# Kernel tuning notes

Hardware: AMD Instinct MI355X
Metric: run time of the kernel (lower is better)

Reference implementation:

```python
import jax, jax.numpy as jnp
import numpy as np

N_POINTS = 100000
N_EVENTS = 1000000
N_PAIRS = 100000      # node_pair_samples
N_RIEMANN = 128       # riemann_samples
INIT_BETA = 0.025
NON_EVENT_W = 1.0
EPS = 1e-6            # torch PairwiseDistance default eps (added to the difference)


def setup_inputs() -> dict:
    key = jax.random.key(0)
    ks = jax.random.split(key, 8)
    # learned parameters
    beta = jnp.full((1, 1), INIT_BETA, jnp.float32)
    z0 = jax.random.uniform(ks[0], (N_POINTS, 2), jnp.float32, -0.025, 0.025)
    v0 = jax.random.uniform(ks[1], (N_POINTS, 2), jnp.float32, -0.025, 0.025)
    a0 = jnp.zeros((N_POINTS, 2), jnp.float32)  # a0 is referenced by step(); zero -> constant-velocity
    # event data: (u, v, event_time)
    u = jax.random.randint(ks[2], (N_EVENTS,), 0, N_POINTS)
    v = jax.random.randint(ks[3], (N_EVENTS,), 0, N_POINTS)
    event_times = jax.random.uniform(ks[4], (N_EVENTS,), jnp.float32, 0.0, 1.0)
    # sampled non-event node pairs (stand-in for randperm over triu indices)
    pair_u = jax.random.randint(ks[5], (N_PAIRS,), 0, N_POINTS)
    pair_v = jax.random.randint(ks[6], (N_PAIRS,), 0, N_POINTS)
    pair_v = jnp.where(pair_v == pair_u, (pair_v + 1) % N_POINTS, pair_v)
    t0 = jnp.float32(0.0)
    tn = jnp.float32(1.0)
    return {"beta": beta, "z0": z0, "v0": v0, "a0": a0,
            "u": u, "v": v, "event_times": event_times,
            "pair_u": pair_u, "pair_v": pair_v, "t0": t0, "tn": tn}


def reference(beta, z0, v0, a0, u, v, event_times, pair_u, pair_v, t0, tn):
    b = beta[0, 0]
    # ---- event intensity: sum_e (beta - ||z_u(t_e) - z_v(t_e)||) ----
    te = event_times[:, None]                                  # [E,1]
    zu = z0[u] + v0[u] * te + 0.5 * a0[u] * te ** 2            # [E,2]
    zv = z0[v] + v0[v] * te + 0.5 * a0[v] * te ** 2            # [E,2]
    d_ev = jnp.sqrt(jnp.sum((zu - zv + EPS) ** 2, axis=-1))    # [E]
    event_intensity = b * event_times.shape[0] - jnp.sum(d_ev)
    # ---- non-event intensity: Riemann sum of exp(beta - d(t)) over sampled pairs ----
    ts = t0 + (jnp.arange(N_RIEMANN, dtype=jnp.float32) / N_RIEMANN) * (tn - t0)  # [T] left Riemann
    dt = (tn - t0) / N_RIEMANN
    dz = z0[pair_u] - z0[pair_v]                               # [P,2]
    dv = v0[pair_u] - v0[pair_v]
    da = a0[pair_u] - a0[pair_v]
    tt = ts[None, :, None]                                     # [1,T,1]
    diff = dz[:, None, :] + dv[:, None, :] * tt + 0.5 * da[:, None, :] * tt ** 2 + EPS  # [P,T,2]
    d_ne = jnp.sqrt(jnp.sum(diff ** 2, axis=-1))               # [P,T]
    non_event_intensity = jnp.sum(jnp.exp(b - d_ne)) * dt
    return event_intensity - NON_EVENT_W * non_event_intensity
```

## Files before the change

### kernel.cpp

```cpp
#include <hip/hip_runtime.h>
#include <hip/hip_fp16.h>

#define N_POINTS   100000
#define N_EVENTS   1000000
#define N_PAIRS    100000
#define N_RIEMANN  128
#define EPS_F      1e-6f
#define NON_EVENT_W 1.0f

constexpr int BLOCK       = 256;
constexpr int EVPT        = 8;
constexpr int EV_THREADS  = N_EVENTS / EVPT;
constexpr int EV_BLOCKS   = (EV_THREADS + BLOCK - 1) / BLOCK;
constexpr int PAIR_BLOCKS = (N_PAIRS + BLOCK - 1) / BLOCK;
constexpr int MAIN_BLOCKS = PAIR_BLOCKS + EV_BLOCKS;
constexpr int PREP_BLOCKS = (N_POINTS + BLOCK - 1) / BLOCK;


__device__ __forceinline__ float block_reduce_sum(float v) {
    #pragma unroll
    for (int off = 32; off > 0; off >>= 1)
        v += __shfl_down(v, off, 64);
    __shared__ float smem[BLOCK / 64];
    const int lane = threadIdx.x & 63;
    const int wid  = threadIdx.x >> 6;
    if (lane == 0) smem[wid] = v;
    __syncthreads();
    float r = 0.f;
    if (threadIdx.x == 0) {
        #pragma unroll
        for (int i = 0; i < BLOCK / 64; ++i) r += smem[i];
    }
    return r;
}

__device__ __forceinline__ void decode_rec(const float4& r, float2& z, float2& v, float2& a) {
    z = __half22float2(*reinterpret_cast<const __half2*>(&r.x));
    v = __half22float2(*reinterpret_cast<const __half2*>(&r.y));
    a = __half22float2(*reinterpret_cast<const __half2*>(&r.z));
}

__global__ __launch_bounds__(BLOCK) void prep_kernel(
    const float2* __restrict__ z0,
    const float2* __restrict__ v0,
    const float2* __restrict__ a0,
    float4*       __restrict__ pts)
{
    const int i = blockIdx.x * BLOCK + threadIdx.x;
    if (i < N_POINTS) {
        const float2 z = z0[i], v = v0[i], a = a0[i];
        float4 r;
        *reinterpret_cast<__half2*>(&r.x) = __float22half2_rn(make_float2(z.x, z.y));
        *reinterpret_cast<__half2*>(&r.y) = __float22half2_rn(make_float2(v.x, v.y));
        *reinterpret_cast<__half2*>(&r.z) = __float22half2_rn(make_float2(a.x, a.y));
        r.w = 0.f;
        pts[i] = r;
    }
}

template <bool PACKED>
__global__ __launch_bounds__(BLOCK) void main_kernel(
    const float4* __restrict__ pts,
    const float2* __restrict__ z0,
    const float2* __restrict__ v0,
    const float2* __restrict__ a0,
    const float*  __restrict__ beta,
    const int*    __restrict__ eu,
    const int*    __restrict__ ev,
    const float*  __restrict__ et,
    const int*    __restrict__ pu,
    const int*    __restrict__ pv,
    const float*  __restrict__ t0p,
    const float*  __restrict__ tnp,
    float*        __restrict__ partials)
{
    float acc = 0.f;
    const int b = blockIdx.x;

    if (b < PAIR_BLOCKS) {
        const int p = b * BLOCK + threadIdx.x;
        if (p < N_PAIRS) {
            const float t0v = t0p[0];
            const float tnv = tnp[0];
            const float dt  = (tnv - t0v) * (1.0f / N_RIEMANN);
            const float bb  = beta[0];
            const int iu = pu[p];
            const int iv = pv[p];
            float dzx, dzy, dvx, dvy, dax, day;
            if (PACKED) {
                const float4 ru = pts[iu];
                const float4 rv = pts[iv];
                float2 zu, vu, au, zv, vv, av;
                decode_rec(ru, zu, vu, au);
                decode_rec(rv, zv, vv, av);
                dzx = zu.x - zv.x; dzy = zu.y - zv.y;
                dvx = vu.x - vv.x; dvy = vu.y - vv.y;
                dax = au.x - av.x; day = au.y - av.y;
            } else {
                const float2 zu = z0[iu], zv = z0[iv];
                const float2 vu = v0[iu], vv = v0[iv];
                const float2 au = a0[iu], av = a0[iv];
                dzx = zu.x - zv.x; dzy = zu.y - zv.y;
                dvx = vu.x - vv.x; dvy = vu.y - vv.y;
                dax = au.x - av.x; day = au.y - av.y;
            }
            const float eb = __expf(bb);
            float s = 0.f;
            #pragma unroll 4
            for (int k = 0; k < N_RIEMANN; ++k) {
                const float t = t0v + (float)k * (1.0f / N_RIEMANN) * (tnv - t0v);
                const float h = 0.5f * t * t;
                const float dx = dzx + dvx * t + dax * h + EPS_F;
                const float dy = dzy + dvy * t + day * h + EPS_F;
                s += __expf(-sqrtf(dx * dx + dy * dy));
            }
            acc = -NON_EVENT_W * dt * eb * s;
        }
    } else {
        const int t = (b - PAIR_BLOCKS) * BLOCK + threadIdx.x;
        if (t < EV_THREADS) {
            const int4*   eu4 = reinterpret_cast<const int4*>(eu);
            const int4*   ev4 = reinterpret_cast<const int4*>(ev);
            const float4* et4 = reinterpret_cast<const float4*>(et);
            const int4 u0 = eu4[2 * t], u1 = eu4[2 * t + 1];
            const int4 w0 = ev4[2 * t], w1 = ev4[2 * t + 1];
            const float4 t0q = et4[2 * t], t1q = et4[2 * t + 1];
            const int iu[EVPT] = { u0.x, u0.y, u0.z, u0.w, u1.x, u1.y, u1.z, u1.w };
            const int iv[EVPT] = { w0.x, w0.y, w0.z, w0.w, w1.x, w1.y, w1.z, w1.w };
            const float te[EVPT] = { t0q.x, t0q.y, t0q.z, t0q.w, t1q.x, t1q.y, t1q.z, t1q.w };
            if (PACKED) {
                float4 ru[EVPT], rv[EVPT];
                #pragma unroll
                for (int j = 0; j < EVPT; ++j) ru[j] = pts[iu[j]];
                #pragma unroll
                for (int j = 0; j < EVPT; ++j) rv[j] = pts[iv[j]];
                #pragma unroll
                for (int j = 0; j < EVPT; ++j) {
                    float2 zu, vu, au, zv, vv, av;
                    decode_rec(ru[j], zu, vu, au);
                    decode_rec(rv[j], zv, vv, av);
                    const float h = 0.5f * te[j] * te[j];
                    const float dx = (zu.x - zv.x) + (vu.x - vv.x) * te[j] + (au.x - av.x) * h + EPS_F;
                    const float dy = (zu.y - zv.y) + (vu.y - vv.y) * te[j] + (au.y - av.y) * h + EPS_F;
                    acc -= sqrtf(dx * dx + dy * dy);
                }
            } else {
                #pragma unroll
                for (int j = 0; j < EVPT; ++j) {
                    const float2 zu = z0[iu[j]], zv = z0[iv[j]];
                    const float2 vu = v0[iu[j]], vv = v0[iv[j]];
                    const float2 au = a0[iu[j]], av = a0[iv[j]];
                    const float h = 0.5f * te[j] * te[j];
                    const float dx = (zu.x - zv.x) + (vu.x - vv.x) * te[j] + (au.x - av.x) * h + EPS_F;
                    const float dy = (zu.y - zv.y) + (vu.y - vv.y) * te[j] + (au.y - av.y) * h + EPS_F;
                    acc -= sqrtf(dx * dx + dy * dy);
                }
            }
        }
    }

    const float r = block_reduce_sum(acc);
    if (threadIdx.x == 0) partials[blockIdx.x] = r;
}

__global__ __launch_bounds__(BLOCK) void reduce_kernel(
    const float* __restrict__ partials,
    const float* __restrict__ beta,
    float*       __restrict__ out)
{
    float acc = 0.f;
    for (int i = threadIdx.x; i < MAIN_BLOCKS; i += BLOCK) acc += partials[i];
    const float r = block_reduce_sum(acc);
    if (threadIdx.x == 0) out[0] = beta[0] * (float)N_EVENTS + r;
}

extern "C" void kernel_launch(void* const* d_in, const int* in_sizes, int n_in,
                              void* d_out, int out_size, void* d_ws, size_t ws_size,
                              hipStream_t stream) {
    const float*  beta = (const float*)d_in[0];
    const float2* z0   = (const float2*)d_in[1];
    const float2* v0   = (const float2*)d_in[2];
    const float2* a0   = (const float2*)d_in[3];
    const int*    eu   = (const int*)d_in[4];
    const int*    ev   = (const int*)d_in[5];
    const float*  et   = (const float*)d_in[6];
    const int*    pu   = (const int*)d_in[7];
    const int*    pv   = (const int*)d_in[8];
    const float*  t0p  = (const float*)d_in[9];
    const float*  tnp  = (const float*)d_in[10];

    float* out = (float*)d_out;
    const size_t pts_bytes = (size_t)N_POINTS * sizeof(float4);
    const bool packed = (ws_size >= pts_bytes + (size_t)MAIN_BLOCKS * sizeof(float));

    if (packed) {
        float4* pts      = (float4*)d_ws;
        float*  partials = (float*)((char*)d_ws + pts_bytes);
        prep_kernel<<<PREP_BLOCKS, BLOCK, 0, stream>>>(z0, v0, a0, pts);
        main_kernel<true><<<MAIN_BLOCKS, BLOCK, 0, stream>>>(
            pts, z0, v0, a0, beta, eu, ev, et, pu, pv, t0p, tnp, partials);
        reduce_kernel<<<1, BLOCK, 0, stream>>>(partials, beta, out);
    } else {
        float* partials = (float*)d_ws;
        main_kernel<false><<<MAIN_BLOCKS, BLOCK, 0, stream>>>(
            nullptr, z0, v0, a0, beta, eu, ev, et, pu, pv, t0p, tnp, partials);
        reduce_kernel<<<1, BLOCK, 0, stream>>>(partials, beta, out);
    }
}
```

Measured before the change: 104.9 us.

## Split Riemann sum across chunk threads and use raw hardware sqrt

Each sampled pair's 128-step Riemann loop is now split into four 32-step chunks handled by separate threads. This gives four times more pair threads, shortens the serial loop behind the block tail, and raises occupancy. The inner loop is rewritten with explicit FMAs, pre-added epsilon and pre-halved acceleration, and it, like the event path, uses the raw amdgcn sqrt instead of the IEEE-correct sqrtf. In exchange, each pair's endpoint records are gathered four times, and the hardware sqrt drops the correction steps, which can change results slightly.

```diff
diff --git a/kernel.cpp b/kernel.cpp
--- a/kernel.cpp
+++ b/kernel.cpp
@@ -9,10 +9,16 @@
 #define NON_EVENT_W 1.0f
 
 constexpr int BLOCK       = 256;
+
 constexpr int EVPT        = 8;
 constexpr int EV_THREADS  = N_EVENTS / EVPT;
 constexpr int EV_BLOCKS   = (EV_THREADS + BLOCK - 1) / BLOCK;
-constexpr int PAIR_BLOCKS = (N_PAIRS + BLOCK - 1) / BLOCK;
+
+constexpr int RPT          = 32;
+constexpr int CHUNKS       = N_RIEMANN / RPT;
+constexpr int PAIR_THREADS = N_PAIRS * CHUNKS;
+constexpr int PAIR_BLOCKS  = (PAIR_THREADS + BLOCK - 1) / BLOCK;
+
 constexpr int MAIN_BLOCKS = PAIR_BLOCKS + EV_BLOCKS;
 constexpr int PREP_BLOCKS = (N_POINTS + BLOCK - 1) / BLOCK;
 
@@ -79,13 +85,15 @@
 
     if (b < PAIR_BLOCKS) {
         const int p = b * BLOCK + threadIdx.x;
-        if (p < N_PAIRS) {
+        if (p < PAIR_THREADS) {
+            const int chunk = p / N_PAIRS;
+            const int pr    = p - chunk * N_PAIRS;
             const float t0v = t0p[0];
             const float tnv = tnp[0];
-            const float dt  = (tnv - t0v) * (1.0f / N_RIEMANN);
+            const float step = (tnv - t0v) * (1.0f / N_RIEMANN);
             const float bb  = beta[0];
-            const int iu = pu[p];
-            const int iv = pv[p];
+            const int iu = pu[pr];
+            const int iv = pv[pr];
             float dzx, dzy, dvx, dvy, dax, day;
             if (PACKED) {
                 const float4 ru = pts[iu];
@@ -104,17 +112,23 @@
                 dvx = vu.x - vv.x; dvy = vu.y - vv.y;
                 dax = au.x - av.x; day = au.y - av.y;
             }
+            const float dzxe = dzx + EPS_F;
+            const float dzye = dzy + EPS_F;
+            const float hax  = 0.5f * dax;
+            const float hay  = 0.5f * day;
             const float eb = __expf(bb);
             float s = 0.f;
-            #pragma unroll 4
-            for (int k = 0; k < N_RIEMANN; ++k) {
-                const float t = t0v + (float)k * (1.0f / N_RIEMANN) * (tnv - t0v);
-                const float h = 0.5f * t * t;
-                const float dx = dzx + dvx * t + dax * h + EPS_F;
-                const float dy = dzy + dvy * t + day * h + EPS_F;
-                s += __expf(-sqrtf(dx * dx + dy * dy));
+            const int k0 = chunk * RPT;
+            #pragma unroll 8
+            for (int k = k0; k < k0 + RPT; ++k) {
+                const float t  = __fmaf_rn((float)k, step, t0v);
+                const float h  = t * t;
+                const float dx = __fmaf_rn(hax, h, __fmaf_rn(dvx, t, dzxe));
+                const float dy = __fmaf_rn(hay, h, __fmaf_rn(dvy, t, dzye));
+                const float d  = __builtin_amdgcn_sqrtf(__fmaf_rn(dy, dy, dx * dx));
+                s += __expf(-d);
             }
-            acc = -NON_EVENT_W * dt * eb * s;
+            acc = -NON_EVENT_W * step * eb * s;
         }
     } else {
         const int t = (b - PAIR_BLOCKS) * BLOCK + threadIdx.x;
@@ -142,7 +156,7 @@
                     const float h = 0.5f * te[j] * te[j];
                     const float dx = (zu.x - zv.x) + (vu.x - vv.x) * te[j] + (au.x - av.x) * h + EPS_F;
                     const float dy = (zu.y - zv.y) + (vu.y - vv.y) * te[j] + (au.y - av.y) * h + EPS_F;
-                    acc -= sqrtf(dx * dx + dy * dy);
+                    acc -= __builtin_amdgcn_sqrtf(__fmaf_rn(dy, dy, dx * dx));
                 }
             } else {
                 #pragma unroll
@@ -153,7 +167,7 @@
                     const float h = 0.5f * te[j] * te[j];
                     const float dx = (zu.x - zv.x) + (vu.x - vv.x) * te[j] + (au.x - av.x) * h + EPS_F;
                     const float dy = (zu.y - zv.y) + (vu.y - vv.y) * te[j] + (au.y - av.y) * h + EPS_F;
-                    acc -= sqrtf(dx * dx + dy * dy);
+                    acc -= __builtin_amdgcn_sqrtf(__fmaf_rn(dy, dy, dx * dx));
                 }
             }
         }
```

New measurement: 101.8 us. -3.0%, faster.
